# Kernel optimization log

Hardware: AMD Instinct MI355X
Metric: run time of the kernel (lower is better)

Reference implementation:

```python
import jax, jax.numpy as jnp
import numpy as np

B, L, DM = 2, 4096, 1024
DI = 2048      # expand * d_model
DT = 64        # dt_rank = ceil(d_model/16)
K = 4          # d_conv


def _silu(v):
    return v * jax.nn.sigmoid(v)


def setup_inputs() -> dict:
    key = jax.random.key(0)
    ks = jax.random.split(key, 9)
    s = lambda k, shape, sc: jax.random.normal(k, shape, dtype=jnp.float32) * sc
    return {
        "x": s(ks[0], (B, L, DM), 1.0),
        "in_proj_w": s(ks[1], (2 * DI, DM), 0.02),
        "conv_w": s(ks[2], (DI, 1, K), 0.1),   # depthwise: [out=DI, in/groups=1, k]
        "conv_b": s(ks[3], (DI,), 0.02),
        "x_proj_w": s(ks[4], (DT, DI), 0.02),
        "dt_proj_w": s(ks[5], (DI, DT), 0.02),
        "dt_proj_b": s(ks[6], (DI,), 0.02),
        "A_log": jax.random.uniform(ks[7], (DI,), jnp.float32, -3.0, -1.0),
        "D": jnp.ones((DI,), jnp.float32),
        "out_proj_w": s(ks[8], (DM, DI), 0.02),
    }


def reference(x, in_proj_w, conv_w, conv_b, x_proj_w, dt_proj_w, dt_proj_b,
              A_log, D, out_proj_w):
    b, l, _ = x.shape
    # input projection and gate split
    xz = jnp.einsum('bld,ed->ble', x, in_proj_w)          # [b,l,2*DI]
    xi, z = jnp.split(xz, 2, axis=-1)                     # each [b,l,DI]
    # depthwise causal conv1d (torch: padding=K-1 both sides, keep first L)
    xc = jnp.transpose(xi, (0, 2, 1))                     # [b,DI,l]
    xc = jax.lax.conv_general_dilated(
        xc, conv_w, window_strides=(1,), padding=[(K - 1, 0)],
        dimension_numbers=('NCH', 'OIH', 'NCH'),
        feature_group_count=xc.shape[1])
    xc = xc + conv_b[None, :, None]
    xi = _silu(jnp.transpose(xc, (0, 2, 1)))              # [b,l,DI]
    # dt path: x_proj -> dt_rank, dt_proj -> d_inner, softplus + clamp
    dt_low = jnp.einsum('bld,rd->blr', xi, x_proj_w)      # [b,l,DT]
    delta = jax.nn.softplus(jnp.einsum('blr,dr->bld', dt_low, dt_proj_w) + dt_proj_b)
    delta = jnp.clip(delta, 1e-6, 10.0)                   # [b,l,DI]
    A = jnp.clip(-jnp.exp(A_log), -10.0, -1e-6)           # [DI]
    e = jnp.clip(jnp.exp(delta * A), 1e-6, 1.0)           # decay factors [b,l,DI]

    # selective scan: state = clip(state*e + u)
    def step(state, eu):
        et, ut = eu
        state = jnp.clip(state * et + ut, -1e4, 1e4)
        return state, state

    init = jnp.zeros((b, xi.shape[-1]), xi.dtype)
    _, states = jax.lax.scan(step, init,
                             (jnp.swapaxes(e, 0, 1), jnp.swapaxes(xi, 0, 1)))
    y = jnp.swapaxes(states, 0, 1) + xi * D               # skip connection
    y = jnp.clip(y, -1e4, 1e4)
    y = y * _silu(z)                                      # gate
    return jnp.einsum('bld,ed->ble', y, out_proj_w)       # [b,l,DM]
```

## Files before the change

### kernel.cpp

```cpp
#include <hip/hip_runtime.h>
#include <cstdint>
#include <cstddef>

#define B_   2
#define L_   4096
#define DM_  1024
#define DI_  2048
#define DT_  64
#define M_   (B_*L_)
#define G_   64
#define CH_  (L_/G_)
#define KSPL 8
#define KSL  (DI_/KSPL)
#define BK_  32
#define LDC  136
#define LDCF 68
#define LDC3 132

typedef __bf16 bf16;
typedef __bf16 bf16x8 __attribute__((ext_vector_type(8)));
typedef __bf16 bf16x4 __attribute__((ext_vector_type(4)));
typedef float  f32x4  __attribute__((ext_vector_type(4)));

__device__ __forceinline__ float silu_f(float x){ return x / (1.f + __expf(-x)); }
__device__ __forceinline__ float softplus_f(float x){
  return fmaxf(x, 0.f) + __logf(1.f + __expf(-fabsf(x)));
}
__device__ __forceinline__ float e_of(float delta, float Ad){
  float ee = __expf(delta * Ad);
  return fminf(fmaxf(ee, 1e-6f), 1.f);
}
__device__ __forceinline__ float a_of(const float* alog, int d){
  float Ad = -__expf(alog[d]);
  return fminf(fmaxf(Ad, -10.f), -1e-6f);
}

__device__ __forceinline__ void gl_lds16(const bf16* g, bf16* l){
  __builtin_amdgcn_global_load_lds(
      (const __attribute__((address_space(1))) void*)g,
      (__attribute__((address_space(3))) void*)l, 16, 0, 0);
}

__device__ __forceinline__ void ds_read128(bf16x8& d, uint32_t addr){
  asm volatile("ds_read_b128 %0, %1" : "=v"(d) : "v"(addr));
}

__global__ __launch_bounds__(256)
void cvt_all_kernel(const float4* __restrict__ s0, bf16x4* __restrict__ d0, int n0,
                    const float4* __restrict__ s1, bf16x4* __restrict__ d1, int n1,
                    const float4* __restrict__ s2, bf16x4* __restrict__ d2, int n2,
                    const float4* __restrict__ s3, bf16x4* __restrict__ d3, int n3,
                    const float4* __restrict__ s4, bf16x4* __restrict__ d4, int n4)
{
  int i = blockIdx.x*256 + threadIdx.x;
  const float4* s; bf16x4* d;
  if      (i < n0)                 { s = s0; d = d0; }
  else if ((i -= n0) < n1)         { s = s1; d = d1; }
  else if ((i -= n1) < n2)         { s = s2; d = d2; }
  else if ((i -= n2) < n3)         { s = s3; d = d3; }
  else if ((i -= n3) < n4)         { s = s4; d = d4; }
  else return;
  float4 v = s[i];
  bf16x4 o = {(bf16)v.x, (bf16)v.y, (bf16)v.z, (bf16)v.w};
  d[i] = o;
}

template<int OUT, int MT, int NT, int KT>
__global__ __launch_bounds__(512, 2)
void gemm256(const bf16* __restrict__ A, const bf16* __restrict__ W,
             bf16* __restrict__ ob, bf16* __restrict__ ob2,
             float* __restrict__ of)
{
  __shared__ __align__(16) char smem[131072];
  char* lA = smem;
  char* lB = smem + 65536;

  const int t    = threadIdx.x;
  const int lane = t & 63;
  const int wave = t >> 6;
  const int wm   = wave >> 2;
  const int wn   = wave & 3;
  const int l16  = lane & 15, quad = lane >> 4;

  const int nnt = NT / 256;
  const int nwg = (MT/256) * nnt;
  const int cpx = nwg >> 3;
  int lin = (blockIdx.x & 7) * cpx + (blockIdx.x >> 3);
  const int m0 = (lin / nnt) * 256;
  const int n0 = (lin % nnt) * 256;

  const int r8     = lane >> 3;
  const int lchunk = (lane & 7) ^ r8;
  const bf16* ap[4]; const bf16* bp[4];
  #pragma unroll
  for (int s = 0; s < 4; ++s){
    ap[s] = A + (size_t)(m0 + s*64 + wave*8 + r8) * KT + lchunk*8;
    bp[s] = W + (size_t)(n0 + s*64 + wave*8 + r8) * KT + lchunk*8;
  }

  auto stage = [&](int ub){
    #pragma unroll
    for (int s = 0; s < 4; ++s){
      gl_lds16(ap[s], (bf16*)(lA + ub*32768 + s*8192 + wave*1024));
      ap[s] += 64;
    }
    #pragma unroll
    for (int s = 0; s < 4; ++s){
      gl_lds16(bp[s], (bf16*)(lB + ub*32768 + s*8192 + wave*1024));
      bp[s] += 64;
    }
  };

  const uint32_t lAu = (uint32_t)(uintptr_t)(__attribute__((address_space(3))) char*)lA;
  const uint32_t lBu = (uint32_t)(uintptr_t)(__attribute__((address_space(3))) char*)lB;
  const uint32_t swz0 = (uint32_t)(((quad    ) ^ (l16 & 7)) << 4);
  const uint32_t swz1 = (uint32_t)(((4 | quad) ^ (l16 & 7)) << 4);
  const uint32_t aB0 = lAu + (uint32_t)((wm*128 + l16) * 128) + swz0;
  const uint32_t aB1 = lAu + (uint32_t)((wm*128 + l16) * 128) + swz1;
  const uint32_t bB0 = lBu + (uint32_t)((wn*64  + l16) * 128) + swz0;
  const uint32_t bB1 = lBu + (uint32_t)((wn*64  + l16) * 128) + swz1;

  f32x4 acc[8][4] = {};
  constexpr int NTILES = KT / 64;

  stage(0);
  for (int tt = 0; tt < NTILES; ++tt){
    const int u = tt & 1;
    if (tt + 1 < NTILES){
      stage(u ^ 1);
      asm volatile("s_waitcnt vmcnt(8)" ::: "memory");
    } else {
      asm volatile("s_waitcnt vmcnt(0)" ::: "memory");
    }
    __builtin_amdgcn_s_barrier();
    __builtin_amdgcn_sched_barrier(0);
    const uint32_t ub = (uint32_t)(u << 15);

    bf16x8 a0[8], a1[8], b0[4], b1[4];
    #pragma unroll
    for (int mi = 0; mi < 8; ++mi) ds_read128(a0[mi], aB0 + ub + mi*2048);
    #pragma unroll
    for (int ni = 0; ni < 4; ++ni) ds_read128(b0[ni], bB0 + ub + ni*2048);
    #pragma unroll
    for (int mi = 0; mi < 8; ++mi) ds_read128(a1[mi], aB1 + ub + mi*2048);
    #pragma unroll
    for (int ni = 0; ni < 4; ++ni) ds_read128(b1[ni], bB1 + ub + ni*2048);

    asm volatile("s_waitcnt lgkmcnt(12)" ::: "memory");
    __builtin_amdgcn_sched_barrier(0);
    __builtin_amdgcn_s_setprio(1);
    #pragma unroll
    for (int mi = 0; mi < 8; ++mi)
      #pragma unroll
      for (int ni = 0; ni < 4; ++ni)
        acc[mi][ni] = __builtin_amdgcn_mfma_f32_16x16x32_bf16(
            a0[mi], b0[ni], acc[mi][ni], 0, 0, 0);
    __builtin_amdgcn_s_setprio(0);
    asm volatile("s_waitcnt lgkmcnt(0)" ::: "memory");
    __builtin_amdgcn_sched_barrier(0);
    __builtin_amdgcn_s_setprio(1);
    #pragma unroll
    for (int mi = 0; mi < 8; ++mi)
      #pragma unroll
      for (int ni = 0; ni < 4; ++ni)
        acc[mi][ni] = __builtin_amdgcn_mfma_f32_16x16x32_bf16(
            a1[mi], b1[ni], acc[mi][ni], 0, 0, 0);
    __builtin_amdgcn_s_setprio(0);
    __builtin_amdgcn_sched_barrier(0);
    __builtin_amdgcn_s_barrier();
  }

  if (OUT == 3){
    float* Cf = (float*)smem;
    #pragma unroll
    for (int pass = 0; pass < 4; ++pass){
      if (wm == (pass >> 1)){
        #pragma unroll
        for (int mi2 = 0; mi2 < 4; ++mi2){
          const int mi = (pass & 1)*4 + mi2;
          #pragma unroll
          for (int ni = 0; ni < 4; ++ni)
            #pragma unroll
            for (int r = 0; r < 4; ++r)
              Cf[(mi2*16 + quad*4 + r)*264 + wn*64 + ni*16 + l16] = acc[mi][ni][r];
        }
      }
      __syncthreads();
      #pragma unroll
      for (int it = 0; it < 8; ++it){
        const int row = it*8 + (t >> 6);
        const int c4  = (t & 63) * 4;
        float4 v = *(const float4*)&Cf[row*264 + c4];
        *(float4*)&of[(size_t)(m0 + pass*64 + row)*NT + n0 + c4] = v;
      }
      __syncthreads();
    }
  } else {
    bf16* Cs = (bf16*)smem;
    const bool isg  = (n0 >= DI_);
    bf16* outp      = isg ? ob2 : ob;
    const int ncol0 = isg ? (n0 - DI_) : n0;
    #pragma unroll
    for (int pass = 0; pass < 2; ++pass){
      if (wm == pass){
        #pragma unroll
        for (int mi = 0; mi < 8; ++mi)
          #pragma unroll
          for (int ni = 0; ni < 4; ++ni)
            #pragma unroll
            for (int r = 0; r < 4; ++r){
              float v = acc[mi][ni][r];
              if (isg) v = silu_f(v);
              Cs[(mi*16 + quad*4 + r)*264 + wn*64 + ni*16 + l16] = (bf16)v;
            }
      }
      __syncthreads();
      #pragma unroll
      for (int it = 0; it < 8; ++it){
        const int row = it*16 + (t >> 5);
        const int c8  = (t & 31) * 8;
        bf16x8 v = *(const bf16x8*)&Cs[row*264 + c8];
        *(bf16x8*)&outp[(size_t)(m0 + pass*128 + row)*DI_ + ncol0 + c8] = v;
      }
      __syncthreads();
    }
  }
}

template<int EPI, int MT, int NT, int KT>
__global__ __launch_bounds__(256)
void gemm_bt(const bf16* __restrict__ A, const bf16* __restrict__ W,
             float* __restrict__ o0, bf16* __restrict__ ob, bf16* __restrict__ ob2,
             const float* __restrict__ bias, const float* __restrict__ alog,
             const bf16* __restrict__ uq, float* __restrict__ Pq,
             float* __restrict__ Fq)
{
  __shared__ char smem[34816];
  bf16* As = (bf16*)smem;
  bf16* Bs = (bf16*)(smem + 128*BK_*2);
  const int t    = threadIdx.x;
  const int lane = t & 63;
  const int wave = t >> 6;
  const int wm   = wave >> 1, wn = wave & 1;
  const int l16  = lane & 15, quad = lane >> 4;

  int m0, n0;
  if (EPI == 4){
    m0 = blockIdx.y * 128; n0 = 0;
  } else {
    const int gx  = NT / 128;
    const int lin = blockIdx.y * gx + blockIdx.x;
    const int grp = lin / (gx * 4);
    const int rem = lin % (gx * 4);
    m0 = (grp * 4 + (rem & 3)) * 128;
    n0 = (rem >> 2) * 128;
  }

  const int srow = (lane >> 2);
  const int scol = (lane & 3) * 8;

  const int KFULL = (EPI == 4) ? (KT * KSPL) : KT;
  const int kbase = (EPI == 4) ? (int)blockIdx.z * KT : 0;

  const int rowA0 = m0 + wave*32 + srow;
  int rB0 = n0 + wave*32 + srow, rB1 = rB0 + 16;
  if (NT < 128){ rB0 = (rB0 >= NT) ? NT-1 : rB0; rB1 = (rB1 >= NT) ? NT-1 : rB1; }
  const bf16* ap0 = A + (size_t)rowA0*KFULL        + kbase + scol;
  const bf16* ap1 = A + (size_t)(rowA0+16)*KFULL   + kbase + scol;
  const bf16* bp0 = W + (size_t)rB0*KFULL          + kbase + scol;
  const bf16* bp1 = W + (size_t)rB1*KFULL          + kbase + scol;
  bf16* lA0 = &As[(wave*32)*BK_];
  bf16* lA1 = &As[(wave*32+16)*BK_];
  bf16* lB0 = &Bs[(wave*32)*BK_];
  bf16* lB1 = &Bs[(wave*32+16)*BK_];

  f32x4 acc[4][4] = {};
  constexpr int kframes = KT / BK_;

  for (int kt = 0; kt < kframes; ++kt){
    gl_lds16(ap0, lA0);  gl_lds16(ap1, lA1);
    gl_lds16(bp0, lB0);  gl_lds16(bp1, lB1);
    ap0 += BK_; ap1 += BK_; bp0 += BK_; bp1 += BK_;
    __syncthreads();
    bf16x8 af[4], bf_[4];
    #pragma unroll
    for (int i = 0; i < 4; ++i){
      af[i]  = *(const bf16x8*)&As[(wm*64 + i*16 + l16)*BK_ + quad*8];
      bf_[i] = *(const bf16x8*)&Bs[(wn*64 + i*16 + l16)*BK_ + quad*8];
    }
    #pragma unroll
    for (int mi = 0; mi < 4; ++mi)
      #pragma unroll
      for (int ni = 0; ni < 4; ++ni)
        acc[mi][ni] = __builtin_amdgcn_mfma_f32_16x16x32_bf16(af[mi], bf_[ni], acc[mi][ni], 0, 0, 0);
    __syncthreads();
  }

  if (EPI == 4){
    float* Cf = (float*)smem;
    if (wn == 0){
      #pragma unroll
      for (int mi = 0; mi < 4; ++mi)
        #pragma unroll
        for (int ni = 0; ni < 4; ++ni)
          #pragma unroll
          for (int r = 0; r < 4; ++r)
            Cf[(wm*64 + mi*16 + quad*4 + r)*LDCF + ni*16 + l16] = acc[mi][ni][r];
    }
    __syncthreads();
    #pragma unroll
    for (int it = 0; it < 8; ++it){
      const int row = it*16 + (t >> 4);
      const int c4  = (t & 15) * 4;
      float4 v = *(const float4*)&Cf[row*LDCF + c4];
      *(float4*)&o0[((size_t)blockIdx.z*M_ + m0 + row)*DT_ + c4] = v;
    }
  } else {
    bf16* Cs = (bf16*)smem;
    #pragma unroll
    for (int mi = 0; mi < 4; ++mi){
      #pragma unroll
      for (int ni = 0; ni < 4; ++ni){
        const int n = n0 + wn*64 + ni*16 + l16;
        #pragma unroll
        for (int r = 0; r < 4; ++r){
          float v = acc[mi][ni][r];
          v = softplus_f(v + bias[n]);
          v = fminf(fmaxf(v, 1e-6f), 10.f);
          Cs[(wm*64 + mi*16 + quad*4 + r)*LDC + wn*64 + ni*16 + l16] = (bf16)v;
        }
      }
    }
    __syncthreads();
    #pragma unroll
    for (int it = 0; it < 8; ++it){
      const int row = it*16 + (t >> 4);
      const int c8  = (t & 15) * 8;
      bf16x8 v = *(const bf16x8*)&Cs[row*LDC + c8];
      *(bf16x8*)&ob[(size_t)(m0+row)*NT + n0 + c8] = v;
    }
    {
      const int chunk = t >> 7;
      const int dcol  = t & 127;
      const int dglob = n0 + dcol;
      const float Ad  = a_of(alog, dglob);
      const int b  = m0 >> 12;
      const int c0 = (m0 & 4095) >> 6;
      const size_t ubase = (size_t)(m0 + chunk*64)*DI_ + dglob;
      float p = 1.f, f = 0.f;
      for (int i = 0; i < CH_; ++i){
        float dl = (float)Cs[(chunk*64 + i)*LDC + dcol];
        float ee = e_of(dl, Ad);
        float uu = (float)uq[ubase + (size_t)i*DI_];
        f = f*ee + uu;
        p *= ee;
      }
      const size_t o = ((size_t)(b*G_ + c0 + chunk))*DI_ + dglob;
      Pq[o] = p; Fq[o] = f;
    }
  }
}

__global__ __launch_bounds__(256)
void dt_reduce_kernel(const float* __restrict__ part, bf16* __restrict__ dtl){
  const int i = blockIdx.x*256 + threadIdx.x;
  float s = 0.f;
  #pragma unroll
  for (int z = 0; z < KSPL; ++z) s += part[(size_t)z*M_*DT_ + i];
  dtl[i] = (bf16)s;
}

__global__ __launch_bounds__(256)
void conv_silu_kernel(const bf16* __restrict__ xi, const float* __restrict__ cw,
                      const float* __restrict__ cb, bf16* __restrict__ ubf)
{
  const int idx = blockIdx.x*256 + threadIdx.x;
  const int d = idx & (DI_-1);
  const int l = (idx >> 11) & (L_-1);
  float s = cb[d];
  #pragma unroll
  for (int k = 0; k < 4; ++k){
    const int ll = l + k - 3;
    if (ll >= 0) s += (float)xi[idx + (k-3)*DI_] * cw[d*4 + k];
  }
  ubf[idx] = (bf16)silu_f(s);
}

__global__ __launch_bounds__(256)
void scan_pass3(const bf16* __restrict__ delta, const bf16* __restrict__ u,
                const bf16* __restrict__ g, const float* __restrict__ P,
                const float* __restrict__ F, const float* __restrict__ alog,
                const float* __restrict__ Dp, bf16* __restrict__ y)
{
  const int d = blockIdx.x*256 + threadIdx.x;
  const int c = blockIdx.y, b = blockIdx.z;
  const float Ad = a_of(alog, d);
  float s = 0.f;
  for (int cc = 0; cc < c; ++cc){
    const size_t o = ((size_t)(b*G_ + cc))*DI_ + d;
    s = F[o] + P[o]*s;
  }
  size_t base = ((size_t)(b*L_ + c*CH_))*DI_ + d;
  const float Dd = Dp[d];
  for (int i = 0; i < CH_; ++i){
    const size_t idx = base + (size_t)i*DI_;
    const float uu = (float)u[idx];
    s = s*e_of((float)delta[idx], Ad) + uu;
    float yy = s + uu*Dd;
    yy = fminf(fmaxf(yy, -1e4f), 1e4f);
    yy *= (float)g[idx];
    y[idx] = (bf16)yy;
  }
}

extern "C" void kernel_launch(void* const* d_in, const int* in_sizes, int n_in,
                              void* d_out, int out_size, void* d_ws, size_t ws_size,
                              hipStream_t stream)
{
  (void)in_sizes; (void)n_in; (void)out_size; (void)ws_size;
  const float* x        = (const float*)d_in[0];
  const float* in_w     = (const float*)d_in[1];
  const float* conv_w   = (const float*)d_in[2];
  const float* conv_b   = (const float*)d_in[3];
  const float* xproj_w  = (const float*)d_in[4];
  const float* dtproj_w = (const float*)d_in[5];
  const float* dtproj_b = (const float*)d_in[6];
  const float* A_log    = (const float*)d_in[7];
  const float* Dp       = (const float*)d_in[8];
  const float* out_w    = (const float*)d_in[9];

  char* base = (char*)d_ws;
  const size_t MiB = 1024*1024;
  bf16*  xi_bf = (bf16*) (base + 0);
  float* part  = (float*)(base + 0);
  bf16*  dl_bf = (bf16*) (base + 0);
  bf16*  x_bf  = (bf16*) (base + 32*MiB);
  bf16*  w1_bf = (bf16*) (base + 48*MiB);
  bf16*  g_bf  = (bf16*) (base + 64*MiB);
  bf16*  u_bf  = (bf16*) (base + 96*MiB);
  bf16*  y_bf  = (bf16*) (base + 128*MiB);
  bf16*  wo_bf = (bf16*) (base + 160*MiB);
  bf16*  xp_bf = (bf16*) (base + 164*MiB);
  bf16*  dp_bf = (bf16*) (base + 165*MiB);
  bf16*  dtl_bf= (bf16*) (base + 166*MiB);
  float* P     = (float*)(base + 167*MiB);
  float* F     = (float*)(base + 168*MiB);

  const int c0 = (M_*DM_)/4, c1 = (2*DI_*DM_)/4, c2 = (DT_*DI_)/4,
            c3 = (DI_*DT_)/4, c4 = (DM_*DI_)/4;
  const int ctot = c0+c1+c2+c3+c4;
  cvt_all_kernel<<<(ctot+255)/256, 256, 0, stream>>>(
      (const float4*)x,        (bf16x4*)x_bf,  c0,
      (const float4*)in_w,     (bf16x4*)w1_bf, c1,
      (const float4*)xproj_w,  (bf16x4*)xp_bf, c2,
      (const float4*)dtproj_w, (bf16x4*)dp_bf, c3,
      (const float4*)out_w,    (bf16x4*)wo_bf, c4);

  gemm256<0, M_, 2*DI_, DM_><<<dim3((M_/256)*((2*DI_)/256)), 512, 0, stream>>>(
      x_bf, w1_bf, xi_bf, g_bf, nullptr);
  conv_silu_kernel<<<(M_*DI_)/256, 256, 0, stream>>>(xi_bf, conv_w, conv_b, u_bf);
  gemm_bt<4, M_, DT_, KSL><<<dim3(1, M_/128, KSPL), 256, 0, stream>>>(
      u_bf, xp_bf, part, nullptr, nullptr, nullptr,
      nullptr, nullptr, nullptr, nullptr);
  dt_reduce_kernel<<<(M_*DT_)/256, 256, 0, stream>>>(part, dtl_bf);
  gemm_bt<2, M_, DI_, DT_><<<dim3(DI_/128, M_/128), 256, 0, stream>>>(
      dtl_bf, dp_bf, nullptr, dl_bf, nullptr, dtproj_b,
      A_log, u_bf, P, F);
  scan_pass3<<<dim3(DI_/256, G_, B_), 256, 0, stream>>>(
      dl_bf, u_bf, g_bf, P, F, A_log, Dp, y_bf);
  gemm256<3, M_, DM_, DI_><<<dim3((M_/256)*(DM_/256)), 512, 0, stream>>>(
      y_bf, wo_bf, nullptr, nullptr, (float*)d_out);
}
```

Measured before the change: 413.3 us.

## Split GEMM K-tile into four quadrant phases interleaving global prefetch with MFMA

Restructures the main GEMM loop of the 256x256 tile kernel into four quadrant sub-phases, each doing a few LDS reads, issuing part of the next tile's global-to-LDS loads, then running a 4x2 block of MFMAs. This replaces the single bulk stage-then-compute pattern, with the aim of spreading memory traffic across the compute and hiding load latency, in the style of a ping-pong schedule. It adds more barriers per iteration and depends on fine-grained vmcnt waits, which risks extra synchronization stalls or ordering hazards if the counts are wrong.

```diff
diff --git a/kernel.cpp b/kernel.cpp
--- a/kernel.cpp
+++ b/kernel.cpp
@@ -98,19 +98,6 @@
     bp[s] = W + (size_t)(n0 + s*64 + wave*8 + r8) * KT + lchunk*8;
   }
 
-  auto stage = [&](int ub){
-    #pragma unroll
-    for (int s = 0; s < 4; ++s){
-      gl_lds16(ap[s], (bf16*)(lA + ub*32768 + s*8192 + wave*1024));
-      ap[s] += 64;
-    }
-    #pragma unroll
-    for (int s = 0; s < 4; ++s){
-      gl_lds16(bp[s], (bf16*)(lB + ub*32768 + s*8192 + wave*1024));
-      bp[s] += 64;
-    }
-  };
-
   const uint32_t lAu = (uint32_t)(uintptr_t)(__attribute__((address_space(3))) char*)lA;
   const uint32_t lBu = (uint32_t)(uintptr_t)(__attribute__((address_space(3))) char*)lB;
   const uint32_t swz0 = (uint32_t)(((quad    ) ^ (l16 & 7)) << 4);
@@ -123,50 +110,132 @@
   f32x4 acc[8][4] = {};
   constexpr int NTILES = KT / 64;
 
-  stage(0);
+  gl_lds16(bp[0], (bf16*)(lB + 0*8192 + wave*1024)); bp[0] += 64;
+  gl_lds16(bp[1], (bf16*)(lB + 1*8192 + wave*1024)); bp[1] += 64;
+  gl_lds16(bp[2], (bf16*)(lB + 2*8192 + wave*1024)); bp[2] += 64;
+  gl_lds16(bp[3], (bf16*)(lB + 3*8192 + wave*1024)); bp[3] += 64;
+  gl_lds16(ap[0], (bf16*)(lA + 0*8192 + wave*1024)); ap[0] += 64;
+  gl_lds16(ap[2], (bf16*)(lA + 2*8192 + wave*1024)); ap[2] += 64;
+  gl_lds16(ap[1], (bf16*)(lA + 1*8192 + wave*1024)); ap[1] += 64;
+  gl_lds16(ap[3], (bf16*)(lA + 3*8192 + wave*1024)); ap[3] += 64;
+  asm volatile("s_waitcnt vmcnt(2)" ::: "memory");
+  __builtin_amdgcn_s_barrier();
+
   for (int tt = 0; tt < NTILES; ++tt){
     const int u = tt & 1;
-    if (tt + 1 < NTILES){
-      stage(u ^ 1);
-      asm volatile("s_waitcnt vmcnt(8)" ::: "memory");
-    } else {
-      asm volatile("s_waitcnt vmcnt(0)" ::: "memory");
-    }
-    __builtin_amdgcn_s_barrier();
-    __builtin_amdgcn_sched_barrier(0);
     const uint32_t ub = (uint32_t)(u << 15);
-
-    bf16x8 a0[8], a1[8], b0[4], b1[4];
-    #pragma unroll
-    for (int mi = 0; mi < 8; ++mi) ds_read128(a0[mi], aB0 + ub + mi*2048);
-    #pragma unroll
-    for (int ni = 0; ni < 4; ++ni) ds_read128(b0[ni], bB0 + ub + ni*2048);
-    #pragma unroll
-    for (int mi = 0; mi < 8; ++mi) ds_read128(a1[mi], aB1 + ub + mi*2048);
-    #pragma unroll
-    for (int ni = 0; ni < 4; ++ni) ds_read128(b1[ni], bB1 + ub + ni*2048);
-
-    asm volatile("s_waitcnt lgkmcnt(12)" ::: "memory");
+    char* sA = lA + (u^1)*32768;
+    char* sB = lB + (u^1)*32768;
+    const bool notlast = (tt + 1 < NTILES);
+
+    bf16x8 a0k0[4], a0k1[4], b0k0[2], b0k1[2];
+    #pragma unroll
+    for (int mi = 0; mi < 4; ++mi) ds_read128(a0k0[mi], aB0 + ub + mi*2048);
+    #pragma unroll
+    for (int mi = 0; mi < 4; ++mi) ds_read128(a0k1[mi], aB1 + ub + mi*2048);
+    #pragma unroll
+    for (int ni = 0; ni < 2; ++ni) ds_read128(b0k0[ni], bB0 + ub + ni*2048);
+    #pragma unroll
+    for (int ni = 0; ni < 2; ++ni) ds_read128(b0k1[ni], bB1 + ub + ni*2048);
+    if (notlast){
+      gl_lds16(bp[0], (bf16*)(sB + 0*8192 + wave*1024)); bp[0] += 64;
+      gl_lds16(bp[1], (bf16*)(sB + 1*8192 + wave*1024)); bp[1] += 64;
+    }
+    asm volatile("s_waitcnt lgkmcnt(8)" ::: "memory");
+    __builtin_amdgcn_s_barrier();
+    asm volatile("s_waitcnt lgkmcnt(0)" ::: "memory");
     __builtin_amdgcn_sched_barrier(0);
     __builtin_amdgcn_s_setprio(1);
     #pragma unroll
-    for (int mi = 0; mi < 8; ++mi)
-      #pragma unroll
-      for (int ni = 0; ni < 4; ++ni)
-        acc[mi][ni] = __builtin_amdgcn_mfma_f32_16x16x32_bf16(
-            a0[mi], b0[ni], acc[mi][ni], 0, 0, 0);
+    for (int mi = 0; mi < 4; ++mi)
+      #pragma unroll
+      for (int ni = 0; ni < 2; ++ni)
+        acc[mi][ni] = __builtin_amdgcn_mfma_f32_16x16x32_bf16(a0k0[mi], b0k0[ni], acc[mi][ni], 0, 0, 0);
+    #pragma unroll
+    for (int mi = 0; mi < 4; ++mi)
+      #pragma unroll
+      for (int ni = 0; ni < 2; ++ni)
+        acc[mi][ni] = __builtin_amdgcn_mfma_f32_16x16x32_bf16(a0k1[mi], b0k1[ni], acc[mi][ni], 0, 0, 0);
     __builtin_amdgcn_s_setprio(0);
+    __builtin_amdgcn_sched_barrier(0);
+    __builtin_amdgcn_s_barrier();
+
+    bf16x8 b1k0[2], b1k1[2];
+    #pragma unroll
+    for (int ni = 0; ni < 2; ++ni) ds_read128(b1k0[ni], bB0 + ub + (2+ni)*2048);
+    #pragma unroll
+    for (int ni = 0; ni < 2; ++ni) ds_read128(b1k1[ni], bB1 + ub + (2+ni)*2048);
+    if (notlast){
+      gl_lds16(bp[2], (bf16*)(sB + 2*8192 + wave*1024)); bp[2] += 64;
+      gl_lds16(bp[3], (bf16*)(sB + 3*8192 + wave*1024)); bp[3] += 64;
+    }
+    __builtin_amdgcn_s_barrier();
     asm volatile("s_waitcnt lgkmcnt(0)" ::: "memory");
     __builtin_amdgcn_sched_barrier(0);
     __builtin_amdgcn_s_setprio(1);
     #pragma unroll
-    for (int mi = 0; mi < 8; ++mi)
-      #pragma unroll
-      for (int ni = 0; ni < 4; ++ni)
-        acc[mi][ni] = __builtin_amdgcn_mfma_f32_16x16x32_bf16(
-            a1[mi], b1[ni], acc[mi][ni], 0, 0, 0);
+    for (int mi = 0; mi < 4; ++mi)
+      #pragma unroll
+      for (int ni = 0; ni < 2; ++ni)
+        acc[mi][2+ni] = __builtin_amdgcn_mfma_f32_16x16x32_bf16(a0k0[mi], b1k0[ni], acc[mi][2+ni], 0, 0, 0);
+    #pragma unroll
+    for (int mi = 0; mi < 4; ++mi)
+      #pragma unroll
+      for (int ni = 0; ni < 2; ++ni)
+        acc[mi][2+ni] = __builtin_amdgcn_mfma_f32_16x16x32_bf16(a0k1[mi], b1k1[ni], acc[mi][2+ni], 0, 0, 0);
     __builtin_amdgcn_s_setprio(0);
     __builtin_amdgcn_sched_barrier(0);
+    if (notlast) asm volatile("s_waitcnt vmcnt(4)" ::: "memory");
+    else         asm volatile("s_waitcnt vmcnt(0)" ::: "memory");
+    __builtin_amdgcn_s_barrier();
+
+    bf16x8 a1k0[4], a1k1[4];
+    #pragma unroll
+    for (int mi = 0; mi < 4; ++mi) ds_read128(a1k0[mi], aB0 + ub + (4+mi)*2048);
+    #pragma unroll
+    for (int mi = 0; mi < 4; ++mi) ds_read128(a1k1[mi], aB1 + ub + (4+mi)*2048);
+    if (notlast){
+      gl_lds16(ap[0], (bf16*)(sA + 0*8192 + wave*1024)); ap[0] += 64;
+      gl_lds16(ap[2], (bf16*)(sA + 2*8192 + wave*1024)); ap[2] += 64;
+    }
+    __builtin_amdgcn_s_barrier();
+    asm volatile("s_waitcnt lgkmcnt(0)" ::: "memory");
+    __builtin_amdgcn_sched_barrier(0);
+    __builtin_amdgcn_s_setprio(1);
+    #pragma unroll
+    for (int mi = 0; mi < 4; ++mi)
+      #pragma unroll
+      for (int ni = 0; ni < 2; ++ni)
+        acc[4+mi][2+ni] = __builtin_amdgcn_mfma_f32_16x16x32_bf16(a1k0[mi], b1k0[ni], acc[4+mi][2+ni], 0, 0, 0);
+    #pragma unroll
+    for (int mi = 0; mi < 4; ++mi)
+      #pragma unroll
+      for (int ni = 0; ni < 2; ++ni)
+        acc[4+mi][2+ni] = __builtin_amdgcn_mfma_f32_16x16x32_bf16(a1k1[mi], b1k1[ni], acc[4+mi][2+ni], 0, 0, 0);
+    __builtin_amdgcn_s_setprio(0);
+    __builtin_amdgcn_sched_barrier(0);
+    __builtin_amdgcn_s_barrier();
+
+    if (notlast){
+      gl_lds16(ap[1], (bf16*)(sA + 1*8192 + wave*1024)); ap[1] += 64;
+      gl_lds16(ap[3], (bf16*)(sA + 3*8192 + wave*1024)); ap[3] += 64;
+    }
+    __builtin_amdgcn_s_barrier();
+    __builtin_amdgcn_sched_barrier(0);
+    __builtin_amdgcn_s_setprio(1);
+    #pragma unroll
+    for (int mi = 0; mi < 4; ++mi)
+      #pragma unroll
+      for (int ni = 0; ni < 2; ++ni)
+        acc[4+mi][ni] = __builtin_amdgcn_mfma_f32_16x16x32_bf16(a1k0[mi], b0k0[ni], acc[4+mi][ni], 0, 0, 0);
+    #pragma unroll
+    for (int mi = 0; mi < 4; ++mi)
+      #pragma unroll
+      for (int ni = 0; ni < 2; ++ni)
+        acc[4+mi][ni] = __builtin_amdgcn_mfma_f32_16x16x32_bf16(a1k1[mi], b0k1[ni], acc[4+mi][ni], 0, 0, 0);
+    __builtin_amdgcn_s_setprio(0);
+    __builtin_amdgcn_sched_barrier(0);
+    if (notlast) asm volatile("s_waitcnt vmcnt(2)" ::: "memory");
     __builtin_amdgcn_s_barrier();
   }
 
```

New measurement: 404.5 us. 2.1% less time.
